# Optimization experiments

Measured on AMD Instinct MI355X. Metric: run time of the kernel, lower is better.

## Reference

```python
import jax, jax.numpy as jnp
import numpy as np

D = 256
H = 8
DH = D // H
N_NODES = 2048
N_EDGES = 4096
NEG = -10000.0
LN_EPS = 1e-5


def _layernorm(x, g, b):
    mu = jnp.mean(x, axis=-1, keepdims=True)
    var = jnp.var(x, axis=-1, keepdims=True)
    return (x - mu) * jax.lax.rsqrt(var + LN_EPS) * g + b


def setup_inputs() -> dict:
    key = jax.random.key(0)
    ks = jax.random.split(key, 20)
    s = 0.05
    x = jax.random.normal(ks[0], (N_NODES, D), jnp.float32)
    edge_index = jax.random.randint(ks[1], (2, N_EDGES), 0, N_NODES)
    edge_attr = jax.random.normal(ks[2], (N_EDGES, D), jnp.float32)
    edge_masks = jax.random.bernoulli(ks[3], 0.95, (N_EDGES, N_EDGES))
    return {
        "x": x,
        "edge_index": edge_index,
        "edge_attr": edge_attr,
        "edge_masks": edge_masks,
        # message MLP: Linear(3d, d) -> LeakyReLU(0.2) -> Linear(d, d)
        "W1": jax.random.normal(ks[4], (D, 3 * D), jnp.float32) * s,
        "b1": jnp.zeros((D,), jnp.float32),
        "W2": jax.random.normal(ks[5], (D, D), jnp.float32) * s,
        "b2": jnp.zeros((D,), jnp.float32),
        # MultiheadAttention params
        "in_proj_w": jax.random.normal(ks[6], (3 * D, D), jnp.float32) * s,
        "in_proj_b": jnp.zeros((3 * D,), jnp.float32),
        "out_w": jax.random.normal(ks[7], (D, D), jnp.float32) * s,
        "out_b": jnp.zeros((D,), jnp.float32),
        # GraphConv root weight + bias
        "root": jax.random.normal(ks[8], (D, D), jnp.float32) * s,
        "bias_p": jnp.zeros((D,), jnp.float32),
        # LayerNorms + residual linear
        "ln1_g": jnp.ones((D,), jnp.float32),
        "ln1_b": jnp.zeros((D,), jnp.float32),
        "ln2_g": jnp.ones((D,), jnp.float32),
        "ln2_b": jnp.zeros((D,), jnp.float32),
        "lin_w": jax.random.normal(ks[9], (D, D), jnp.float32) * s,
        "lin_b": jnp.zeros((D,), jnp.float32),
    }


def reference(x, edge_index, edge_attr, edge_masks,
              W1, b1, W2, b2,
              in_proj_w, in_proj_b, out_w, out_b,
              root, bias_p, ln1_g, ln1_b, ln2_g, ln2_b, lin_w, lin_b):
    # --- message: gather endpoints, concat with edge features, MLP ---
    x_j = x[edge_index[0]]            # source [E, d]
    x_i = x[edge_index[1]]            # target [E, d]
    h = jnp.concatenate([x_i, x_j, edge_attr], axis=1)          # [E, 3d]
    h = jax.nn.leaky_relu(h @ W1.T + b1, negative_slope=0.2)
    h = h @ W2.T + b2                                            # [E, d]

    # --- MultiheadAttention over edges (L=E, batch=1), eval mode ---
    qkv = h @ in_proj_w.T + in_proj_b                            # [E, 3d]
    q, k, v = jnp.split(qkv, 3, axis=1)
    q = q.reshape(N_EDGES, H, DH).transpose(1, 0, 2)             # [H, E, dh]
    k = k.reshape(N_EDGES, H, DH).transpose(1, 0, 2)
    v = v.reshape(N_EDGES, H, DH).transpose(1, 0, 2)
    scores = jnp.einsum('hed,hfd->hef', q, k) / np.sqrt(DH)      # [H, E, E]
    add_mask = jnp.where(edge_masks, 0.0, NEG).astype(scores.dtype)
    attn = jax.nn.softmax(scores + add_mask[None], axis=-1)
    o = jnp.einsum('hef,hfd->hed', attn, v)                      # [H, E, dh]
    o = o.transpose(1, 0, 2).reshape(N_EDGES, D)
    msg = o @ out_w.T + out_b                                    # [E, d]

    # --- scatter-add aggregation to target nodes + update ---
    aggr = jax.ops.segment_sum(msg, edge_index[1], num_segments=N_NODES)
    out = aggr + x @ root + bias_p                               # [N, d]

    # --- graph_block: norm1 -> residual linear -> norm2 ---
    y = _layernorm(out, ln1_g, ln1_b)
    y = _layernorm(y + (y @ lin_w.T + lin_b), ln2_g, ln2_b)
    return y
```

## Files before the change

### kernel.cpp

```cpp
#include <hip/hip_runtime.h>
#include <hip/hip_bf16.h>
#include <cstdint>

#define D_   256
#define E_   4096
#define NN_  2048

typedef float f32x4_t __attribute__((ext_vector_type(4)));
typedef short bf16x8_t __attribute__((ext_vector_type(8)));

__device__ inline short f2bf(float f) {
    union { float fv; unsigned u; } v; v.fv = f;
    unsigned r = v.u + 0x7fffu + ((v.u >> 16) & 1u);
    return (short)(r >> 16);
}

__device__ inline unsigned cvtpk_bf16(float lo, float hi) {
    unsigned r;
    asm("v_cvt_pk_bf16_f32 %0, %1, %2" : "=v"(r) : "v"(lo), "v"(hi));
    return r;
}

template<int ACT, bool GATHER, bool SCATTER, bool HASADD, bool OBF16>
__global__ __launch_bounds__(256)
void mgemm_k(const float* __restrict__ A, const float* __restrict__ Bm,
             const float* __restrict__ bias, const float* __restrict__ addsrc,
             float* __restrict__ C, int M, int N, int K,
             const int* __restrict__ ei0, const int* __restrict__ ei1,
             const float* __restrict__ x, const float* __restrict__ eattr,
             float qsc)
{
    __shared__ char lds[16384];
    const int tid = threadIdx.x;
    const int w = tid >> 6, l = tid & 63;
    const int g = l >> 4, ln = l & 15;
    const int wr = w >> 1, wc = w & 1;
    const int m0 = blockIdx.x * 64, n0 = blockIdx.y * 64;

    const int srow = tid >> 2;
    const int sck  = (tid & 3) * 8;
    const int sswz = (srow & 7) << 4;
    int gi1 = 0, gi0 = 0;
    if (GATHER) { gi1 = ei1[m0 + srow]; gi0 = ei0[m0 + srow]; }

    f32x4_t acc[2][2];
    #pragma unroll
    for (int m = 0; m < 2; m++)
        #pragma unroll
        for (int n = 0; n < 2; n++)
            acc[m][n] = f32x4_t{0.f, 0.f, 0.f, 0.f};

    const int nt = K >> 5;
    float4 ga0, ga1, gb0, gb1;

    auto loadG = [&](int kk) {
        const int cb = kk + sck;
        const float* src;
        if (GATHER) {
            if (cb < 256)      src = x + (size_t)gi1 * 256 + cb;
            else if (cb < 512) src = x + (size_t)gi0 * 256 + (cb - 256);
            else               src = eattr + (size_t)(m0 + srow) * 256 + (cb - 512);
        } else {
            src = A + (size_t)(m0 + srow) * K + cb;
        }
        ga0 = *(const float4*)src;
        ga1 = *(const float4*)(src + 4);
        const float* bsrc = Bm + (size_t)(n0 + srow) * K + cb;
        gb0 = *(const float4*)bsrc;
        gb1 = *(const float4*)(bsrc + 4);
    };
    auto writeS = [&](int buf) {
        uint4 pa, pb;
        pa.x = cvtpk_bf16(ga0.x, ga0.y); pa.y = cvtpk_bf16(ga0.z, ga0.w);
        pa.z = cvtpk_bf16(ga1.x, ga1.y); pa.w = cvtpk_bf16(ga1.z, ga1.w);
        pb.x = cvtpk_bf16(gb0.x, gb0.y); pb.y = cvtpk_bf16(gb0.z, gb0.w);
        pb.z = cvtpk_bf16(gb1.x, gb1.y); pb.w = cvtpk_bf16(gb1.z, gb1.w);
        const int off = (srow*64 + sck*2) ^ sswz;
        *(uint4*)(lds + buf*4096 + off) = pa;
        *(uint4*)(lds + 8192 + buf*4096 + off) = pb;
    };

    loadG(0);
    writeS(0);
    __syncthreads();
    int cur = 0;
    for (int t = 0; t < nt; ++t) {
        if (t + 1 < nt) loadG((t + 1) << 5);
        bf16x8_t af[2], bfr[2];
        #pragma unroll
        for (int m = 0; m < 2; m++) {
            const int row = wr*32 + m*16 + ln;
            af[m] = *(const bf16x8_t*)(lds + cur*4096 + ((row*64 + g*16) ^ ((row&7)<<4)));
        }
        #pragma unroll
        for (int n = 0; n < 2; n++) {
            const int row = wc*32 + n*16 + ln;
            bfr[n] = *(const bf16x8_t*)(lds + 8192 + cur*4096 + ((row*64 + g*16) ^ ((row&7)<<4)));
        }
        #pragma unroll
        for (int m = 0; m < 2; m++)
            #pragma unroll
            for (int n = 0; n < 2; n++)
                acc[m][n] = __builtin_amdgcn_mfma_f32_16x16x32_bf16(af[m], bfr[n], acc[m][n], 0, 0, 0);
        if (t + 1 < nt) writeS(cur ^ 1);
        __syncthreads();
        cur ^= 1;
    }

    #pragma unroll
    for (int m = 0; m < 2; m++) {
        #pragma unroll
        for (int n = 0; n < 2; n++) {
            const int col = n0 + wc*32 + n*16 + ln;
            const float bv = bias[col];
            #pragma unroll
            for (int r = 0; r < 4; r++) {
                const int row = m0 + wr*32 + m*16 + g*4 + r;
                float v = acc[m][n][r] + bv;
                if (ACT == 1) v = v > 0.f ? v : 0.2f * v;
                if (HASADD) v += addsrc[(size_t)row * N + col];
                if (SCATTER) {
                    atomicAdd(&C[(size_t)ei1[row] * 256 + col], v);
                } else if (OBF16) {
                    ((short*)C)[(size_t)row * N + col] = f2bf((col < 256) ? v * qsc : v);
                } else {
                    C[(size_t)row * N + col] = v;
                }
            }
        }
    }
}

__global__ __launch_bounds__(256)
void prep_k(const int* __restrict__ mraw, unsigned int* __restrict__ pm,
            const float* __restrict__ root, float* __restrict__ rootT,
            float* __restrict__ aggr)
{
    __shared__ float T[64][65];
    const int bid = blockIdx.x;
    if (bid < 2048) {
        const int t = bid * 256 + threadIdx.x;
        aggr[t] = 0.f;
        const int row = t >> 7, wb = t & 127;
        unsigned int bits = 0;
        const uint4* p = (const uint4*)(mraw + (size_t)row * 4096 + wb * 32);
        #pragma unroll
        for (int g = 0; g < 8; g++) {
            const uint4 v = p[g];
            if (v.x) bits |= 1u << (g*4+0);
            if (v.y) bits |= 1u << (g*4+1);
            if (v.z) bits |= 1u << (g*4+2);
            if (v.w) bits |= 1u << (g*4+3);
        }
        pm[t] = bits;
    } else {
        const int bt = bid - 2048;
        const int m0 = (bt >> 2) * 64, n0 = (bt & 3) * 64;
        const int r = threadIdx.x >> 6, c = threadIdx.x & 63;
        #pragma unroll
        for (int i = 0; i < 16; i++)
            T[r + i*4][c] = root[(size_t)(m0 + r + i*4) * 256 + n0 + c];
        __syncthreads();
        #pragma unroll
        for (int i = 0; i < 16; i++)
            rootT[(size_t)(n0 + r + i*4) * 256 + m0 + c] = T[c][r + i*4];
    }
}

__global__ __launch_bounds__(256)
void vtrans_k(const short* __restrict__ qkvb, short* __restrict__ vt)
{
    __shared__ short Ts[64][40];
    const int head = blockIdx.x >> 6;
    const int k0 = (blockIdx.x & 63) * 64;
    const int tid = threadIdx.x;
    const int skey = tid >> 2, sc = tid & 3;
    const bf16x8_t v = *(const bf16x8_t*)(qkvb + (size_t)(k0 + skey)*768 + 512 + head*32 + sc*8);
    *(bf16x8_t*)(&Ts[skey][sc*8]) = v;
    __syncthreads();
    const int sd = tid >> 3, skc = tid & 7;
    short outv[8];
    #pragma unroll
    for (int j = 0; j < 8; j++) outv[j] = Ts[skc*8 + j][sd];
    *(bf16x8_t*)(vt + (size_t)head*131072 + (size_t)sd*4096 + k0 + skc*8) = *(bf16x8_t*)outv;
}

__global__ __launch_bounds__(512, 4)
void attn_k(const short* __restrict__ qkvb, const short* __restrict__ vt,
            const unsigned int* __restrict__ pmask, float* __restrict__ o)
{
    __shared__ char lds[49152];
    const int tid = threadIdx.x;
    const int w2 = tid >> 6, l = tid & 63;
    const int g = l >> 4, ln = l & 15;
    const int gi = w2 >> 2, wq = w2 & 3;
    const int head = blockIdx.x >> 6;
    const int q0 = (blockIdx.x & 63) * 64;
    const int qa = q0 + wq * 16 + ln;

    const bf16x8_t qf = *(const bf16x8_t*)(qkvb + (size_t)qa*768 + head*32 + g*8);

    f32x4_t oT0 = {0.f,0.f,0.f,0.f};
    f32x4_t oT1 = {0.f,0.f,0.f,0.f};
    float lsum = 0.f;

    const int st = tid & 255;
    const int skey = st >> 2, sc = st & 3;
    const int sd = st >> 3, skc = st & 7;
    const short* kgp = qkvb + 256 + head*32 + sc*8;
    const short* vgp = vt + (size_t)head*131072 + (size_t)sd*4096 + skc*8;
    char* Kg = lds + gi*8192;
    char* Vg = lds + 16384 + gi*8192;
    char* Pw = lds + 32768 + w2*2048;
    const unsigned int* mrow = pmask + (size_t)qa*128;
    const int kswz = (skey & 7) << 4, vswz = (sd & 7) << 4;
    const int pswz = (ln & 7) << 4;

    uint2 mwc;
    {
        const int k0 = gi * 64;
        const bf16x8_t kv = *(const bf16x8_t*)(kgp + (size_t)(k0 + skey)*768);
        *(bf16x8_t*)(Kg + ((skey*64 + sc*16) ^ kswz)) = kv;
        const bf16x8_t vv = *(const bf16x8_t*)(vgp + k0);
        *(bf16x8_t*)(Vg + ((sd*128 + skc*16) ^ vswz)) = vv;
        mwc = *(const uint2*)(mrow + gi*2);
    }

    for (int i = 0; i < 32; ++i) {
        __syncthreads();
        const int cur = i & 1;
        const int tt = 2*i + gi;
        uint2 mwn;
        if (i < 31) {
            const int k0n = (tt + 2) * 64;
            const bf16x8_t kv = *(const bf16x8_t*)(kgp + (size_t)(k0n + skey)*768);
            *(bf16x8_t*)(Kg + (cur^1)*4096 + ((skey*64 + sc*16) ^ kswz)) = kv;
            const bf16x8_t vv = *(const bf16x8_t*)(vgp + k0n);
            *(bf16x8_t*)(Vg + (cur^1)*4096 + ((sd*128 + skc*16) ^ vswz)) = vv;
            mwn = *(const uint2*)(mrow + (tt + 2)*2);
        }
        char* Kb = Kg + cur*4096;
        char* Vb = Vg + cur*4096;

        f32x4_t s[4];
        __builtin_amdgcn_s_setprio(1);
        #pragma unroll
        for (int kt = 0; kt < 4; kt++) {
            const int key = kt*16 + ln;
            const bf16x8_t kf = *(const bf16x8_t*)(Kb + ((key*64 + g*16) ^ ((key & 7) << 4)));
            f32x4_t z = {0.f,0.f,0.f,0.f};
            s[kt] = __builtin_amdgcn_mfma_f32_16x16x32_bf16(kf, qf, z, 0, 0, 0);
        }
        __builtin_amdgcn_s_setprio(0);

        #pragma unroll
        for (int kt = 0; kt < 4; kt++) {
            const unsigned word = (kt < 2) ? mwc.x : mwc.y;
            float p[4];
            #pragma unroll
            for (int r = 0; r < 4; r++) {
                const float e = __expf(s[kt][r] - 12.0f);
                p[r] = ((word >> ((kt & 1)*16 + g*4 + r)) & 1u) ? e : 0.f;
            }
            lsum += (p[0] + p[1]) + (p[2] + p[3]);
            uint2 pk;
            pk.x = cvtpk_bf16(p[0], p[1]);
            pk.y = cvtpk_bf16(p[2], p[3]);
            *(uint2*)(Pw + ((ln*128 + kt*32 + g*8) ^ pswz)) = pk;
        }

        __builtin_amdgcn_s_setprio(1);
        #pragma unroll
        for (int kh = 0; kh < 2; kh++) {
            const bf16x8_t pf = *(const bf16x8_t*)(Pw + ((ln*128 + kh*64 + g*16) ^ pswz));
            const bf16x8_t vf0 = *(const bf16x8_t*)(Vb + ((ln*128 + kh*64 + g*16) ^ pswz));
            const bf16x8_t vf1 = *(const bf16x8_t*)(Vb + (((16+ln)*128 + kh*64 + g*16) ^ pswz));
            oT0 = __builtin_amdgcn_mfma_f32_16x16x32_bf16(vf0, pf, oT0, 0, 0, 0);
            oT1 = __builtin_amdgcn_mfma_f32_16x16x32_bf16(vf1, pf, oT1, 0, 0, 0);
        }
        __builtin_amdgcn_s_setprio(0);
        mwc = mwn;
    }

    __syncthreads();
    *(f32x4_t*)(lds + w2*2048 + l*32)      = oT0;
    *(f32x4_t*)(lds + w2*2048 + l*32 + 16) = oT1;
    ((float*)(lds + 16384))[w2*64 + l] = lsum;
    __syncthreads();
    if (gi == 0) {
        const int pw = w2 + 4;
        const f32x4_t b0 = *(const f32x4_t*)(lds + pw*2048 + l*32);
        const f32x4_t b1 = *(const f32x4_t*)(lds + pw*2048 + l*32 + 16);
        const float lp = ((const float*)(lds + 16384))[pw*64 + l];
        oT0 += b0; oT1 += b1;
        lsum += lp;
        lsum += __shfl_xor(lsum, 16);
        lsum += __shfl_xor(lsum, 32);
        const float inv = 1.0f / fmaxf(lsum, 1e-37f);
        float* op = o + (size_t)qa * 256 + head*32;
        float4 v0 = {oT0[0]*inv, oT0[1]*inv, oT0[2]*inv, oT0[3]*inv};
        float4 v1 = {oT1[0]*inv, oT1[1]*inv, oT1[2]*inv, oT1[3]*inv};
        *(float4*)(op + g*4) = v0;
        *(float4*)(op + 16 + g*4) = v1;
    }
}

__global__ __launch_bounds__(256)
void ln_k(const float* __restrict__ in, const float* __restrict__ g,
          const float* __restrict__ b, float* __restrict__ out)
{
    const int n = blockIdx.x, t = threadIdx.x;
    const float v = in[(size_t)n * 256 + t];
    float s1 = v, s2 = v * v;
    #pragma unroll
    for (int off = 32; off > 0; off >>= 1) {
        s1 += __shfl_xor(s1, off);
        s2 += __shfl_xor(s2, off);
    }
    __shared__ float r1[4], r2[4];
    const int wv = t >> 6;
    if ((t & 63) == 0) { r1[wv] = s1; r2[wv] = s2; }
    __syncthreads();
    const float t1 = r1[0] + r1[1] + r1[2] + r1[3];
    const float t2 = r2[0] + r2[1] + r2[2] + r2[3];
    const float mu  = t1 * (1.0f / 256.0f);
    const float var = t2 * (1.0f / 256.0f) - mu * mu;
    const float rs  = rsqrtf(var + 1e-5f);
    out[(size_t)n * 256 + t] = (v - mu) * rs * g[t] + b[t];
}

extern "C" void kernel_launch(void* const* d_in, const int* in_sizes, int n_in,
                              void* d_out, int out_size, void* d_ws, size_t ws_size,
                              hipStream_t stream)
{
    const float* x     = (const float*)d_in[0];
    const int*   ei    = (const int*)  d_in[1];
    const float* eattr = (const float*)d_in[2];
    const int*   mask  = (const int*)  d_in[3];
    const float* W1   = (const float*)d_in[4];
    const float* b1   = (const float*)d_in[5];
    const float* W2   = (const float*)d_in[6];
    const float* b2   = (const float*)d_in[7];
    const float* ipw  = (const float*)d_in[8];
    const float* ipb  = (const float*)d_in[9];
    const float* ow   = (const float*)d_in[10];
    const float* ob   = (const float*)d_in[11];
    const float* root = (const float*)d_in[12];
    const float* bp   = (const float*)d_in[13];
    const float* ln1g = (const float*)d_in[14];
    const float* ln1b = (const float*)d_in[15];
    const float* ln2g = (const float*)d_in[16];
    const float* ln2b = (const float*)d_in[17];
    const float* linw = (const float*)d_in[18];
    const float* linb = (const float*)d_in[19];
    const int* ei0 = ei;
    const int* ei1 = ei + E_;

    float* ws = (float*)d_ws;
    float* h1    = ws;
    float* h     = ws + 1048576;
    short* qkvb  = (short*)(ws + 2097152);
    float* aggr  = ws + 3670016;
    float* outb  = ws + 4194304;
    unsigned int* pmask = (unsigned int*)(ws + 4718592);
    short* vt    = (short*)(ws + 5242896);
    float* rootT = ws + 5767184;
    float* o    = h1;
    float* y1   = h;
    float* z    = h1;

    dim3 blk(256);
    prep_k<<<dim3(2064), blk, 0, stream>>>(mask, pmask, root, rootT, aggr);

    mgemm_k<1,true,false,false,false><<<dim3(64,4), blk, 0, stream>>>(
        nullptr, W1, b1, nullptr, h1, E_, 256, 768, ei0, ei1, x, eattr, 1.0f);
    mgemm_k<0,false,false,false,false><<<dim3(64,4), blk, 0, stream>>>(
        h1, W2, b2, nullptr, h, E_, 256, 256, nullptr, nullptr, nullptr, nullptr, 1.0f);
    mgemm_k<0,false,false,false,true><<<dim3(64,12), blk, 0, stream>>>(
        h, ipw, ipb, nullptr, (float*)qkvb, E_, 768, 256, nullptr, nullptr, nullptr, nullptr,
        0.17677669529663687f);
    vtrans_k<<<dim3(512), blk, 0, stream>>>(qkvb, vt);
    attn_k<<<dim3(512), dim3(512), 0, stream>>>(qkvb, vt, pmask, o);
    mgemm_k<0,false,true,false,false><<<dim3(64,4), blk, 0, stream>>>(
        o, ow, ob, nullptr, aggr, E_, 256, 256, nullptr, ei1, nullptr, nullptr, 1.0f);
    mgemm_k<0,false,false,true,false><<<dim3(32,4), blk, 0, stream>>>(
        x, rootT, bp, aggr, outb, NN_, 256, 256, nullptr, nullptr, nullptr, nullptr, 1.0f);
    ln_k<<<dim3(2048), blk, 0, stream>>>(outb, ln1g, ln1b, y1);
    mgemm_k<0,false,false,true,false><<<dim3(32,4), blk, 0, stream>>>(
        y1, linw, linb, y1, z, NN_, 256, 256, nullptr, nullptr, nullptr, nullptr, 1.0f);
    ln_k<<<dim3(2048), blk, 0, stream>>>(z, ln2g, ln2b, (float*)d_out);
}
```

Before: 124.8 us.

## Store intermediate GEMM activations as bf16 and fuse V transpose into QKV epilogue

The first two GEMMs now write bf16 activations, and their consumers load bf16 directly, which halves the intermediate traffic and skips a conversion. The QKV GEMM epilogue writes V straight into the per-head transposed layout, so the separate vtrans kernel and its launch are removed. Softmax uses exp2f with the log2(e) factor folded into the q scale, saving a multiply per exponential. In exchange, the h1 intermediate is now rounded to bf16, and the transposed V writes are 8-byte scattered stores.

```diff
diff --git a/kernel.cpp b/kernel.cpp
--- a/kernel.cpp
+++ b/kernel.cpp
@@ -8,6 +8,7 @@
 
 typedef float f32x4_t __attribute__((ext_vector_type(4)));
 typedef short bf16x8_t __attribute__((ext_vector_type(8)));
+typedef short bf16x4_t __attribute__((ext_vector_type(4)));
 
 __device__ inline short f2bf(float f) {
     union { float fv; unsigned u; } v; v.fv = f;
@@ -21,11 +22,12 @@
     return r;
 }
 
-template<int ACT, bool GATHER, bool SCATTER, bool HASADD, bool OBF16>
+template<int ACT, bool GATHER, bool SCATTER, bool HASADD, bool ABF16, int OUT>
 __global__ __launch_bounds__(256)
-void mgemm_k(const float* __restrict__ A, const float* __restrict__ Bm,
+void mgemm_k(const void* __restrict__ A, const float* __restrict__ Bm,
              const float* __restrict__ bias, const float* __restrict__ addsrc,
-             float* __restrict__ C, int M, int N, int K,
+             void* __restrict__ C, short* __restrict__ vtb,
+             int M, int N, int K,
              const int* __restrict__ ei0, const int* __restrict__ ei1,
              const float* __restrict__ x, const float* __restrict__ eattr,
              float qsc)
@@ -52,31 +54,41 @@
 
     const int nt = K >> 5;
     float4 ga0, ga1, gb0, gb1;
+    bf16x8_t gab;
 
     auto loadG = [&](int kk) {
         const int cb = kk + sck;
-        const float* src;
-        if (GATHER) {
-            if (cb < 256)      src = x + (size_t)gi1 * 256 + cb;
-            else if (cb < 512) src = x + (size_t)gi0 * 256 + (cb - 256);
-            else               src = eattr + (size_t)(m0 + srow) * 256 + (cb - 512);
+        if (ABF16) {
+            gab = *(const bf16x8_t*)((const short*)A + (size_t)(m0 + srow) * K + cb);
         } else {
-            src = A + (size_t)(m0 + srow) * K + cb;
-        }
-        ga0 = *(const float4*)src;
-        ga1 = *(const float4*)(src + 4);
+            const float* src;
+            if (GATHER) {
+                if (cb < 256)      src = x + (size_t)gi1 * 256 + cb;
+                else if (cb < 512) src = x + (size_t)gi0 * 256 + (cb - 256);
+                else               src = eattr + (size_t)(m0 + srow) * 256 + (cb - 512);
+            } else {
+                src = (const float*)A + (size_t)(m0 + srow) * K + cb;
+            }
+            ga0 = *(const float4*)src;
+            ga1 = *(const float4*)(src + 4);
+        }
         const float* bsrc = Bm + (size_t)(n0 + srow) * K + cb;
         gb0 = *(const float4*)bsrc;
         gb1 = *(const float4*)(bsrc + 4);
     };
     auto writeS = [&](int buf) {
-        uint4 pa, pb;
-        pa.x = cvtpk_bf16(ga0.x, ga0.y); pa.y = cvtpk_bf16(ga0.z, ga0.w);
-        pa.z = cvtpk_bf16(ga1.x, ga1.y); pa.w = cvtpk_bf16(ga1.z, ga1.w);
+        const int off = (srow*64 + sck*2) ^ sswz;
+        if (ABF16) {
+            *(bf16x8_t*)(lds + buf*4096 + off) = gab;
+        } else {
+            uint4 pa;
+            pa.x = cvtpk_bf16(ga0.x, ga0.y); pa.y = cvtpk_bf16(ga0.z, ga0.w);
+            pa.z = cvtpk_bf16(ga1.x, ga1.y); pa.w = cvtpk_bf16(ga1.z, ga1.w);
+            *(uint4*)(lds + buf*4096 + off) = pa;
+        }
+        uint4 pb;
         pb.x = cvtpk_bf16(gb0.x, gb0.y); pb.y = cvtpk_bf16(gb0.z, gb0.w);
         pb.z = cvtpk_bf16(gb1.x, gb1.y); pb.w = cvtpk_bf16(gb1.z, gb1.w);
-        const int off = (srow*64 + sck*2) ^ sswz;
-        *(uint4*)(lds + buf*4096 + off) = pa;
         *(uint4*)(lds + 8192 + buf*4096 + off) = pb;
     };
 
@@ -113,18 +125,40 @@
         for (int n = 0; n < 2; n++) {
             const int col = n0 + wc*32 + n*16 + ln;
             const float bv = bias[col];
+            const int row0 = m0 + wr*32 + m*16 + g*4;
+            float pv[4];
             #pragma unroll
             for (int r = 0; r < 4; r++) {
-                const int row = m0 + wr*32 + m*16 + g*4 + r;
                 float v = acc[m][n][r] + bv;
                 if (ACT == 1) v = v > 0.f ? v : 0.2f * v;
-                if (HASADD) v += addsrc[(size_t)row * N + col];
-                if (SCATTER) {
-                    atomicAdd(&C[(size_t)ei1[row] * 256 + col], v);
-                } else if (OBF16) {
-                    ((short*)C)[(size_t)row * N + col] = f2bf((col < 256) ? v * qsc : v);
+                if (HASADD) v += addsrc[(size_t)(row0 + r) * N + col];
+                pv[r] = v;
+            }
+            if (SCATTER) {
+                #pragma unroll
+                for (int r = 0; r < 4; r++)
+                    atomicAdd(&((float*)C)[(size_t)ei1[row0 + r] * 256 + col], pv[r]);
+            } else if (OUT == 0) {
+                #pragma unroll
+                for (int r = 0; r < 4; r++)
+                    ((float*)C)[(size_t)(row0 + r) * N + col] = pv[r];
+            } else if (OUT == 1) {
+                #pragma unroll
+                for (int r = 0; r < 4; r++)
+                    ((short*)C)[(size_t)(row0 + r) * N + col] =
+                        f2bf((col < 256) ? pv[r] * qsc : pv[r]);
+            } else {
+                if (col < 512) {
+                    #pragma unroll
+                    for (int r = 0; r < 4; r++)
+                        ((short*)C)[(size_t)(row0 + r) * 768 + col] =
+                            f2bf((col < 256) ? pv[r] * qsc : pv[r]);
                 } else {
-                    C[(size_t)row * N + col] = v;
+                    const int hd = (col - 512) >> 5, d = (col - 512) & 31;
+                    bf16x4_t pk;
+                    #pragma unroll
+                    for (int r = 0; r < 4; r++) pk[r] = f2bf(pv[r]);
+                    *(bf16x4_t*)(vtb + (size_t)hd*131072 + (size_t)d*4096 + row0) = pk;
                 }
             }
         }
@@ -167,24 +201,6 @@
     }
 }
 
-__global__ __launch_bounds__(256)
-void vtrans_k(const short* __restrict__ qkvb, short* __restrict__ vt)
-{
-    __shared__ short Ts[64][40];
-    const int head = blockIdx.x >> 6;
-    const int k0 = (blockIdx.x & 63) * 64;
-    const int tid = threadIdx.x;
-    const int skey = tid >> 2, sc = tid & 3;
-    const bf16x8_t v = *(const bf16x8_t*)(qkvb + (size_t)(k0 + skey)*768 + 512 + head*32 + sc*8);
-    *(bf16x8_t*)(&Ts[skey][sc*8]) = v;
-    __syncthreads();
-    const int sd = tid >> 3, skc = tid & 7;
-    short outv[8];
-    #pragma unroll
-    for (int j = 0; j < 8; j++) outv[j] = Ts[skc*8 + j][sd];
-    *(bf16x8_t*)(vt + (size_t)head*131072 + (size_t)sd*4096 + k0 + skc*8) = *(bf16x8_t*)outv;
-}
-
 __global__ __launch_bounds__(512, 4)
 void attn_k(const short* __restrict__ qkvb, const short* __restrict__ vt,
             const unsigned int* __restrict__ pmask, float* __restrict__ o)
@@ -259,7 +275,7 @@
             float p[4];
             #pragma unroll
             for (int r = 0; r < 4; r++) {
-                const float e = __expf(s[kt][r] - 12.0f);
+                const float e = exp2f(s[kt][r] - 17.312340490667562f);
                 p[r] = ((word >> ((kt & 1)*16 + g*4 + r)) & 1u) ? e : 0.f;
             }
             lsum += (p[0] + p[1]) + (p[2] + p[3]);
@@ -357,36 +373,36 @@
     const int* ei1 = ei + E_;
 
     float* ws = (float*)d_ws;
-    float* h1    = ws;
-    float* h     = ws + 1048576;
+    short* h1b   = (short*)ws;
+    short* hb    = (short*)(ws + 524288);
+    float* o     = ws + 1048576;
+    float* y1    = ws + 1048576;
+    float* z     = ws + 1572864;
     short* qkvb  = (short*)(ws + 2097152);
     float* aggr  = ws + 3670016;
     float* outb  = ws + 4194304;
     unsigned int* pmask = (unsigned int*)(ws + 4718592);
     short* vt    = (short*)(ws + 5242896);
     float* rootT = ws + 5767184;
-    float* o    = h1;
-    float* y1   = h;
-    float* z    = h1;
+
 
     dim3 blk(256);
     prep_k<<<dim3(2064), blk, 0, stream>>>(mask, pmask, root, rootT, aggr);
 
-    mgemm_k<1,true,false,false,false><<<dim3(64,4), blk, 0, stream>>>(
-        nullptr, W1, b1, nullptr, h1, E_, 256, 768, ei0, ei1, x, eattr, 1.0f);
-    mgemm_k<0,false,false,false,false><<<dim3(64,4), blk, 0, stream>>>(
-        h1, W2, b2, nullptr, h, E_, 256, 256, nullptr, nullptr, nullptr, nullptr, 1.0f);
-    mgemm_k<0,false,false,false,true><<<dim3(64,12), blk, 0, stream>>>(
-        h, ipw, ipb, nullptr, (float*)qkvb, E_, 768, 256, nullptr, nullptr, nullptr, nullptr,
-        0.17677669529663687f);
-    vtrans_k<<<dim3(512), blk, 0, stream>>>(qkvb, vt);
+    mgemm_k<1,true,false,false,false,1><<<dim3(64,4), blk, 0, stream>>>(
+        nullptr, W1, b1, nullptr, h1b, nullptr, E_, 256, 768, ei0, ei1, x, eattr, 1.0f);
+    mgemm_k<0,false,false,false,true,1><<<dim3(64,4), blk, 0, stream>>>(
+        h1b, W2, b2, nullptr, hb, nullptr, E_, 256, 256, nullptr, nullptr, nullptr, nullptr, 1.0f);
+    mgemm_k<0,false,false,false,true,2><<<dim3(64,12), blk, 0, stream>>>(
+        hb, ipw, ipb, nullptr, qkvb, vt, E_, 768, 256, nullptr, nullptr, nullptr, nullptr,
+        0.25503486f);
     attn_k<<<dim3(512), dim3(512), 0, stream>>>(qkvb, vt, pmask, o);
-    mgemm_k<0,false,true,false,false><<<dim3(64,4), blk, 0, stream>>>(
-        o, ow, ob, nullptr, aggr, E_, 256, 256, nullptr, ei1, nullptr, nullptr, 1.0f);
-    mgemm_k<0,false,false,true,false><<<dim3(32,4), blk, 0, stream>>>(
-        x, rootT, bp, aggr, outb, NN_, 256, 256, nullptr, nullptr, nullptr, nullptr, 1.0f);
+    mgemm_k<0,false,true,false,false,0><<<dim3(64,4), blk, 0, stream>>>(
+        o, ow, ob, nullptr, aggr, nullptr, E_, 256, 256, nullptr, ei1, nullptr, nullptr, 1.0f);
+    mgemm_k<0,false,false,true,false,0><<<dim3(32,4), blk, 0, stream>>>(
+        x, rootT, bp, aggr, outb, nullptr, NN_, 256, 256, nullptr, nullptr, nullptr, nullptr, 1.0f);
     ln_k<<<dim3(2048), blk, 0, stream>>>(outb, ln1g, ln1b, y1);
-    mgemm_k<0,false,false,true,false><<<dim3(32,4), blk, 0, stream>>>(
-        y1, linw, linb, y1, z, NN_, 256, 256, nullptr, nullptr, nullptr, nullptr, 1.0f);
+    mgemm_k<0,false,false,true,false,0><<<dim3(32,4), blk, 0, stream>>>(
+        y1, linw, linb, y1, z, nullptr, NN_, 256, 256, nullptr, nullptr, nullptr, nullptr, 1.0f);
     ln_k<<<dim3(2048), blk, 0, stream>>>(z, ln2g, ln2b, (float*)d_out);
 }
```

After: 137.6 us. 1.1x slower.
